# Performance work log

Measured on AMD Instinct MI355X. Metric: run time of the kernel, lower is better.

The kernel has to match this reference:

```python
import jax, jax.numpy as jnp
import numpy as np

B = 32      # batch
N = 1024    # input_size (= maxval)
EPS = 1.0   # regularization_strength


def _isotonic_l2(y):
    """Non-increasing isotonic regression (L2) of each row of y: [B, n].

    Uses the minimax characterization  sol_i = min_{j<=i} max_{k>=i} mean(y[j..k]),
    which equals the PAV solution and yields the correct block-averaging Jacobian
    under autodiff. O(n^2) memory per row, fully vectorized.
    """
    b, n = y.shape
    cs = jnp.concatenate([jnp.zeros((b, 1), y.dtype), jnp.cumsum(y, axis=-1)], axis=-1)  # [B, n+1]
    j = jnp.arange(n)[:, None]   # start index
    k = jnp.arange(n)[None, :]   # end index
    length = (k - j + 1).astype(y.dtype)
    # M[b, j, k] = mean(y[b, j..k]) for k >= j
    M = (cs[:, None, 1:] - cs[:, :-1, None]) / jnp.where(k >= j, length, jnp.ones_like(length))
    M = jnp.where(k >= j, M, -jnp.inf)
    # Amax[b, j, i] = max_{k >= i} M[b, j, k]  (suffix max along k)
    Amax = jax.lax.cummax(M, axis=2, reverse=True)
    # restrict to j <= i, then minimize over j
    Amax = jnp.where(j <= k, Amax, jnp.inf)  # here the k-axis plays the role of i
    return jnp.min(Amax, axis=1)  # [B, n]


def _soft_rank(x, eps):
    """fast-soft-sort soft_rank, direction=ASCENDING, regularization='l2'."""
    b, n = x.shape
    theta = x / eps
    perm = jnp.argsort(-theta, axis=-1)                 # descending sort permutation
    s = jnp.take_along_axis(theta, perm, axis=-1)       # sorted (descending)
    w = jnp.arange(n, 0, -1, dtype=x.dtype)             # [n, n-1, ..., 1]
    sol = _isotonic_l2(s - w)                           # dual solution
    primal = s - sol                                    # projection, sorted order
    inv = jnp.argsort(perm, axis=-1)
    return jnp.take_along_axis(primal, inv, axis=-1)    # unpermute -> ranks in [1, n]


def setup_inputs() -> dict:
    key = jax.random.key(0)
    x = jax.random.normal(key, (B, N), dtype=jnp.float32)
    return {"x": x}


def reference(x) -> jnp.ndarray:
    ranks = _soft_rank(x, EPS)                          # [B, n]
    n = x.shape[1]
    t = jnp.arange(1, n + 1, dtype=x.dtype)             # rank targets 1..n
    # out[b, j, i] = relu(1 - |ranks[b, j] - (i + 1)|)  (== torch .permute(0, 2, 1) result)
    return jax.nn.relu(1.0 - jnp.abs(ranks[:, :, None] - t[None, None, :]))
```

## Files before the change

### kernel.cpp

```cpp
#include <hip/hip_runtime.h>
#include <stdint.h>

#define N 1024
#define BATCH 32

__global__ __launch_bounds__(256) void count_kernel(const float* __restrict__ x,
                                                    int* __restrict__ pos_g) {
    __shared__ uint64_t keys[N];
    __shared__ int      partial[256];

    const int row   = blockIdx.x >> 4;
    const int chunk = blockIdx.x & 15;
    const int t     = threadIdx.x;

    const float4 xq = reinterpret_cast<const float4*>(x + row * N)[t];
    {
        const float vv[4] = {xq.x, xq.y, xq.z, xq.w};
        const int j0 = t << 2;
        #pragma unroll
        for (int e = 0; e < 4; ++e) {
            uint32_t u = __float_as_uint(vv[e]);
            u ^= (u & 0x80000000u) ? 0xFFFFFFFFu : 0x80000000u;
            keys[j0 + e] = (((uint64_t)u) << 10) | (uint64_t)(1023 - (j0 + e));
        }
    }
    __syncthreads();

    const int e = (chunk << 6) + (t & 63);
    const int q = t >> 6;
    const uint64_t kk = keys[e];
    const int kbeg = q << 8;
    int c = 0;
    #pragma unroll 4
    for (int k = kbeg; k < kbeg + 256; k += 4) {
        c += (int)(keys[k    ] > kk);
        c += (int)(keys[k + 1] > kk);
        c += (int)(keys[k + 2] > kk);
        c += (int)(keys[k + 3] > kk);
    }
    partial[t] = c;
    __syncthreads();

    if (t < 64)
        pos_g[row * N + e] = partial[t] + partial[t + 64] + partial[t + 128] + partial[t + 192];
}

__global__ __launch_bounds__(256) void ranks_kernel(const float* __restrict__ x,
                                                    const int* __restrict__ pos_g,
                                                    float* __restrict__ ranks) {
    __shared__ float    ss[N];
    __shared__ float    yv[N];
    __shared__ double   csum[N];
    __shared__ int      segid[N];
    __shared__ int      run_start[N+1];
    __shared__ float    run_mean[N];
    __shared__ double   stk_sum[N];
    __shared__ int      stk_cnt[N];
    __shared__ int      stk_runs[N];
    __shared__ double   wsumD[4];
    __shared__ int      wsumI[4];

    const int b = blockIdx.x;
    const int t = threadIdx.x;
    const int j0 = t << 2;
    const int lane = t & 63;
    const int wid = t >> 6;

    const float4 xq = reinterpret_cast<const float4*>(x + b * N)[t];
    const int4   pq = reinterpret_cast<const int4*>(pos_g + b * N)[t];
    ss[pq.x] = xq.x; ss[pq.y] = xq.y; ss[pq.z] = xq.z; ss[pq.w] = xq.w;
    __syncthreads();

    float4 yq;
    {
        const float4 sq = reinterpret_cast<const float4*>(ss)[t];
        yq.x = sq.x + (float)(j0 - 512);
        yq.y = sq.y + (float)(j0 - 511);
        yq.z = sq.z + (float)(j0 - 510);
        yq.w = sq.w + (float)(j0 - 509);
        reinterpret_cast<float4*>(yv)[t] = yq;
    }
    __syncthreads();

    const float ye[4] = {yq.x, yq.y, yq.z, yq.w};
    int    fl[4];
    int    lf[4];
    double lys[4];
    {
        float prev = (j0 == 0) ? -1.0e30f : yv[j0 - 1];
        double accy = 0.0; int accf = 0;
        #pragma unroll
        for (int e = 0; e < 4; ++e) {
            const int f = (prev > ye[e]) ? 1 : 0;
            prev = ye[e];
            fl[e] = f;
            accf += f;             lf[e]  = accf;
            accy += (double)ye[e]; lys[e] = accy;
        }
    }
    double vy = lys[3]; int vf = lf[3];
    #pragma unroll
    for (int off = 1; off < 64; off <<= 1) {
        const double oy = __shfl_up(vy, off);
        const int    of = __shfl_up(vf, off);
        if (lane >= off) { vy += oy; vf += of; }
    }
    if (lane == 63) { wsumD[wid] = vy; wsumI[wid] = vf; }
    __syncthreads();
    {
        double basey = vy - lys[3]; int basef = vf - lf[3];
        for (int w = 0; w < wid; ++w) { basey += wsumD[w]; basef += wsumI[w]; }
        #pragma unroll
        for (int e = 0; e < 4; ++e) {
            const int p   = j0 + e;
            const int seg = basef + lf[e];
            segid[p] = seg;
            csum[p]  = basey + lys[e];
            if (fl[e]) run_start[seg] = p;
        }
        if (t == 0) run_start[0] = 0;
    }
    __syncthreads();

    if (t == 0) {
        const int R = segid[N - 1] + 1;
        run_start[R] = N;
        int sp = 0;
        for (int r = 0; r < R; ++r) {
            const int a   = run_start[r];
            const int bnd = run_start[r + 1];
            double s = csum[bnd - 1] - ((a > 0) ? csum[a - 1] : 0.0);
            int    c = bnd - a;
            int    nr = 1;
            while (sp > 0 && s * (double)stk_cnt[sp - 1] > stk_sum[sp - 1] * (double)c) {
                s  += stk_sum[sp - 1];
                c  += stk_cnt[sp - 1];
                nr += stk_runs[sp - 1];
                --sp;
            }
            stk_sum[sp] = s; stk_cnt[sp] = c; stk_runs[sp] = nr; ++sp;
        }
        int rc = 0;
        for (int e2 = 0; e2 < sp; ++e2) {
            const float m = (float)(stk_sum[e2] / (double)stk_cnt[e2]);
            for (int q2 = 0; q2 < stk_runs[e2]; ++q2) run_mean[rc++] = m;
        }
    }
    __syncthreads();

    float4 r4;
    r4.x = xq.x - run_mean[segid[pq.x]] + 512.0f;
    r4.y = xq.y - run_mean[segid[pq.y]] + 512.0f;
    r4.z = xq.z - run_mean[segid[pq.z]] + 512.0f;
    r4.w = xq.w - run_mean[segid[pq.w]] + 512.0f;
    reinterpret_cast<float4*>(ranks + b * N)[t] = r4;
}

__global__ __launch_bounds__(256) void fill_kernel(const float* __restrict__ ranks,
                                                   float* __restrict__ out) {
    const int r0 = blockIdx.x << 2;
    const int i = threadIdx.x << 2;
    const float ra = ranks[r0 + 0];
    const float rb = ranks[r0 + 1];
    const float rc = ranks[r0 + 2];
    const float rd = ranks[r0 + 3];
    const float rv[4] = {ra, rb, rc, rd};
    #pragma unroll
    for (int rr = 0; rr < 4; ++rr) {
        const float r = rv[rr];
        float4 o;
        o.x = fmaxf(1.0f - fabsf(r - (float)(i + 1)), 0.0f);
        o.y = fmaxf(1.0f - fabsf(r - (float)(i + 2)), 0.0f);
        o.z = fmaxf(1.0f - fabsf(r - (float)(i + 3)), 0.0f);
        o.w = fmaxf(1.0f - fabsf(r - (float)(i + 4)), 0.0f);
        reinterpret_cast<float4*>(out + (size_t)(r0 + rr) * N)[threadIdx.x] = o;
    }
}

extern "C" void kernel_launch(void* const* d_in, const int* in_sizes, int n_in,
                              void* d_out, int out_size, void* d_ws, size_t ws_size,
                              hipStream_t stream) {
    const float* x = (const float*)d_in[0];
    float* out = (float*)d_out;
    int*   pos_g = (int*)d_ws;
    float* ranks = (float*)d_ws + BATCH * N;

    count_kernel<<<BATCH * 16, 256, 0, stream>>>(x, pos_g);
    ranks_kernel<<<BATCH, 256, 0, stream>>>(x, pos_g, ranks);
    fill_kernel<<<(BATCH * N) / 4, 256, 0, stream>>>(ranks, out);
}
```

Baseline: 141.3 us.

## Overlap zero-fill of output with PAV blocks and scatter sparse nonzeros

The dense fill kernel is replaced by extra blocks in the ranks kernel that write zeros over the whole 128MB output while the 32 PAV blocks compute ranks, so the serial isotonic step overlaps the bandwidth-bound store. A small scatter kernel then writes the at most two nonzero entries per row, taken from the floor and fractional part of each rank. This removes the compute and rank reads from the big write pass, but adds a dependency: zeros must land before the scatter, which holds through stream ordering.

```diff
diff --git a/kernel.cpp b/kernel.cpp
--- a/kernel.cpp
+++ b/kernel.cpp
@@ -3,6 +3,7 @@
 
 #define N 1024
 #define BATCH 32
+#define NFILL 4096
 
 __global__ __launch_bounds__(256) void count_kernel(const float* __restrict__ x,
                                                     int* __restrict__ pos_g) {
@@ -45,9 +46,19 @@
         pos_g[row * N + e] = partial[t] + partial[t + 64] + partial[t + 128] + partial[t + 192];
 }
 
-__global__ __launch_bounds__(256) void ranks_kernel(const float* __restrict__ x,
-                                                    const int* __restrict__ pos_g,
-                                                    float* __restrict__ ranks) {
+__global__ __launch_bounds__(256) void fused_ranks_fill(const float* __restrict__ x,
+                                                        const int* __restrict__ pos_g,
+                                                        float* __restrict__ ranks,
+                                                        float* __restrict__ out) {
+    if (blockIdx.x >= BATCH) {
+        const int fid = blockIdx.x - BATCH;
+        float4* o = reinterpret_cast<float4*>(out) + (size_t)fid * 2048 + threadIdx.x;
+        const float4 z = make_float4(0.0f, 0.0f, 0.0f, 0.0f);
+        #pragma unroll
+        for (int i = 0; i < 8; ++i) o[i * 256] = z;
+        return;
+    }
+
     __shared__ float    ss[N];
     __shared__ float    yv[N];
     __shared__ double   csum[N];
@@ -156,25 +167,16 @@
     reinterpret_cast<float4*>(ranks + b * N)[t] = r4;
 }
 
-__global__ __launch_bounds__(256) void fill_kernel(const float* __restrict__ ranks,
-                                                   float* __restrict__ out) {
-    const int r0 = blockIdx.x << 2;
-    const int i = threadIdx.x << 2;
-    const float ra = ranks[r0 + 0];
-    const float rb = ranks[r0 + 1];
-    const float rc = ranks[r0 + 2];
-    const float rd = ranks[r0 + 3];
-    const float rv[4] = {ra, rb, rc, rd};
-    #pragma unroll
-    for (int rr = 0; rr < 4; ++rr) {
-        const float r = rv[rr];
-        float4 o;
-        o.x = fmaxf(1.0f - fabsf(r - (float)(i + 1)), 0.0f);
-        o.y = fmaxf(1.0f - fabsf(r - (float)(i + 2)), 0.0f);
-        o.z = fmaxf(1.0f - fabsf(r - (float)(i + 3)), 0.0f);
-        o.w = fmaxf(1.0f - fabsf(r - (float)(i + 4)), 0.0f);
-        reinterpret_cast<float4*>(out + (size_t)(r0 + rr) * N)[threadIdx.x] = o;
-    }
+__global__ __launch_bounds__(256) void scatter_kernel(const float* __restrict__ ranks,
+                                                      float* __restrict__ out) {
+    const int row = blockIdx.x * 256 + threadIdx.x;
+    const float r = ranks[row];
+    const float f = floorf(r);
+    const int   i1 = (int)f;
+    const float frac = r - f;
+    float* o = out + (size_t)row * N;
+    if (i1 >= 1 && i1 <= N) o[i1 - 1] = 1.0f - frac;
+    if (i1 >= 0 && i1 <  N) o[i1]     = frac;
 }
 
 extern "C" void kernel_launch(void* const* d_in, const int* in_sizes, int n_in,
@@ -186,6 +188,6 @@
     float* ranks = (float*)d_ws + BATCH * N;
 
     count_kernel<<<BATCH * 16, 256, 0, stream>>>(x, pos_g);
-    ranks_kernel<<<BATCH, 256, 0, stream>>>(x, pos_g, ranks);
-    fill_kernel<<<(BATCH * N) / 4, 256, 0, stream>>>(ranks, out);
+    fused_ranks_fill<<<BATCH + NFILL, 256, 0, stream>>>(x, pos_g, ranks, out);
+    scatter_kernel<<<(BATCH * N) / 256, 256, 0, stream>>>(ranks, out);
 }
```

Result: no change. 140.0 us (-0.9%).
